# Kernel optimization log

Measured on AMD Instinct MI355X. Metric: run time of the kernel, lower is better.

The kernel has to match this reference:

```python
import jax, jax.numpy as jnp
import numpy as np

B, N, D, BS = 2, 4096, 2048, 256  # batch, seq, d_model, chunk size


def rms_norm(x):
    eps = jnp.asarray(jnp.finfo(x.dtype).eps, x.dtype)
    return x * jax.lax.rsqrt(jnp.mean(x * x, axis=-1, keepdims=True) + eps)


def la_kernel(q, k, v, bs):
    # chunked linear attention: intra-chunk masked QK^T + cross-chunk KV recurrence
    b, n, d = q.shape
    T = n // bs
    qc = q.reshape(b, T, bs, d).transpose(1, 0, 2, 3)  # [T,B,bs,d]
    kc = k.reshape(b, T, bs, d).transpose(1, 0, 2, 3)
    vc = v.reshape(b, T, bs, d).transpose(1, 0, 2, 3)
    mask = jnp.tril(jnp.ones((bs, bs), q.dtype))

    def step(kv, qkv):
        qt, kt, vt = qkv  # each [B,bs,d]
        s = jnp.einsum('bid,bjd->bij', qt, kt) * mask        # masked intra-chunk scores
        ot = jnp.einsum('bij,bjd->bid', s, vt) + jnp.einsum('bid,bde->bie', qt, kv)
        kv = kv + jnp.einsum('bjd,bje->bde', kt, vt)          # state update AFTER output
        return kv, ot

    kv0 = jnp.zeros((b, d, d), q.dtype)
    _, o = jax.lax.scan(step, kv0, (qc, kc, vc))              # o: [T,B,bs,d]
    return o.transpose(1, 0, 2, 3).reshape(b, n, d)


def setup_inputs() -> dict:
    key = jax.random.key(0)
    ks = jax.random.split(key, 6)
    scale = 0.02
    x = jax.random.normal(ks[0], (B, N, D), jnp.float32)
    Wq = jax.random.normal(ks[1], (D, D), jnp.float32) * scale
    Wk = jax.random.normal(ks[2], (D, D), jnp.float32) * scale
    Wv = jax.random.normal(ks[3], (D, D), jnp.float32) * scale
    Wg = jax.random.normal(ks[4], (D, D), jnp.float32) * scale
    Wp = jax.random.normal(ks[5], (D, D), jnp.float32) * scale
    return {'x': x, 'Wq': Wq, 'Wk': Wk, 'Wv': Wv, 'Wg': Wg, 'Wp': Wp}


def reference(x, Wq, Wk, Wv, Wg, Wp):
    # weights stored torch-style (out,in): y = x @ W^T
    xn = rms_norm(x)
    q = jax.nn.silu(jnp.einsum('bnd,od->bno', xn, Wq))
    k = jax.nn.silu(jnp.einsum('bnd,od->bno', xn, Wk))
    v = jax.nn.silu(jnp.einsum('bnd,od->bno', xn, Wv))
    g = jax.nn.sigmoid(jnp.einsum('bnd,od->bno', xn, Wg))
    o = la_kernel(q, k, v, BS) * g
    return jnp.einsum('bnd,od->bno', o, Wp)
```

## Files before the change

### kernel.cpp

```cpp
#include <hip/hip_runtime.h>
#include <hip/hip_bf16.h>

typedef __bf16 bf16;
typedef __bf16 bf16x4 __attribute__((ext_vector_type(4)));
typedef __bf16 bf16x8 __attribute__((ext_vector_type(8)));
typedef float f32x4 __attribute__((ext_vector_type(4)));
typedef unsigned int u32;

#define D_    2048
#define NSEQ  4096
#define BATCH 2
#define CH    1024
#define TC    4
#define MROWS 8192

__device__ __forceinline__ void gload16(const bf16* g, bf16* l) {
  __builtin_amdgcn_global_load_lds(
      (const __attribute__((address_space(1))) u32*)g,
      (__attribute__((address_space(3))) u32*)l, 16, 0, 0);
}


struct SmemTiles {
  alignas(16) bf16 As[2][128 * 32];
  alignas(16) bf16 Bs[2][128 * 32];
};

__device__ __forceinline__ void stage128(SmemTiles& sm, int bb, const bf16* A,
                                         int lda, const bf16* B, int ldb,
                                         int k0, int tid) {
#pragma unroll
  for (int it = 0; it < 2; ++it) {
    int c = it * 256 + tid;
    int r = c >> 2;
    int co = (c & 3) << 3;
    gload16(A + (size_t)r * lda + k0 + co, &sm.As[bb][c * 8]);
    gload16(B + (size_t)r * ldb + k0 + co, &sm.Bs[bb][c * 8]);
  }
}

__device__ __forceinline__ void gemm_core(SmemTiles& sm, const bf16* A, int lda,
                                          const bf16* B, int ldb, int K,
                                          f32x4 acc[4][4]) {
  const int tid = threadIdx.x;
  const int lane = tid & 63;
  const int wave = tid >> 6;
  const int wr = wave >> 1, wc = wave & 1;
  const int l15 = lane & 15, kl = lane >> 4;
  const int NT = K >> 5;
  if (NT <= 0) return;

  stage128(sm, 0, A, lda, B, ldb, 0, tid);
  __syncthreads();

  const int ao = (wr * 64 + l15) * 32 + kl * 8;
  const int bo = (wc * 64 + l15) * 32 + kl * 8;

  for (int t = 0; t < NT; ++t) {
    if (t + 1 < NT)
      stage128(sm, (t + 1) & 1, A, lda, B, ldb, (t + 1) * 32, tid);
    const bf16* Ab = sm.As[t & 1];
    const bf16* Bb = sm.Bs[t & 1];
    bf16x8 a[4], b[4];
#pragma unroll
    for (int m = 0; m < 4; ++m) a[m] = *(const bf16x8*)(Ab + ao + m * 16 * 32);
#pragma unroll
    for (int n = 0; n < 4; ++n) b[n] = *(const bf16x8*)(Bb + bo + n * 16 * 32);
    __builtin_amdgcn_s_setprio(1);
#pragma unroll
    for (int m = 0; m < 4; ++m)
#pragma unroll
      for (int n = 0; n < 4; ++n)
        acc[m][n] = __builtin_amdgcn_mfma_f32_16x16x32_bf16(a[m], b[n], acc[m][n], 0, 0, 0);
    __builtin_amdgcn_s_setprio(0);
    if (t + 1 < NT) __syncthreads();
  }
}

#define EPILOGUE_VARS                              \
  const int lane = threadIdx.x & 63;               \
  const int wave = threadIdx.x >> 6;               \
  const int wr = wave >> 1, wc = wave & 1;         \
  const int l15 = lane & 15, kl = lane >> 4;


struct SmemW {
  alignas(16) bf16 A[2][128 * 32];
  alignas(16) bf16 B[2][256 * 32];
};

__device__ __forceinline__ void stageW(SmemW& sm, int bb, const bf16* A,
                                       int lda, const bf16* B, int ldb,
                                       int k0, int wave, int lane) {
  const int r16 = lane & 15, c8 = lane >> 4;
  gload16(A + (size_t)(wave * 16 + r16) * lda + k0 + c8 * 8,
          &sm.A[bb][wave * 512 + lane * 8]);
#pragma unroll
  for (int j = 0; j < 2; ++j) {
    int nb = 2 * wave + j;
    gload16(B + (size_t)(nb * 16 + r16) * ldb + k0 + c8 * 8,
            &sm.B[bb][nb * 512 + lane * 8]);
  }
}

__device__ __forceinline__ void gemmW_core(SmemW& sm, const bf16* A, int lda,
                                           const bf16* B, int ldb, int K,
                                           f32x4 acc[4][4]) {
  const int tid = threadIdx.x;
  const int wave = tid >> 6, lane = tid & 63;
  const int wr = wave >> 2, wc = wave & 3;
  const int NT = K >> 5;
  if (NT <= 0) return;

  stageW(sm, 0, A, lda, B, ldb, 0, wave, lane);
  if (NT > 1) {
    stageW(sm, 1, A, lda, B, ldb, 32, wave, lane);
    asm volatile("s_waitcnt vmcnt(3)" ::: "memory");
  } else {
    asm volatile("s_waitcnt vmcnt(0)" ::: "memory");
  }
  __builtin_amdgcn_s_barrier();

  const int aoff = wr * 2048 + lane * 8;
  const int boff = wc * 2048 + lane * 8;

  for (int t = 0; t < NT; ++t) {
    const bf16* Ab = sm.A[t & 1];
    const bf16* Bb = sm.B[t & 1];
    bf16x8 av[4], bv[4];
#pragma unroll
    for (int m = 0; m < 4; ++m) av[m] = *(const bf16x8*)&Ab[aoff + m * 512];
#pragma unroll
    for (int n = 0; n < 4; ++n) bv[n] = *(const bf16x8*)&Bb[boff + n * 512];
    asm volatile("s_waitcnt lgkmcnt(0)" ::: "memory");
    __builtin_amdgcn_s_barrier();
    if (t + 2 < NT)
      stageW(sm, t & 1, A, lda, B, ldb, (t + 2) * 32, wave, lane);
    __builtin_amdgcn_s_setprio(1);
#pragma unroll
    for (int m = 0; m < 4; ++m)
#pragma unroll
      for (int n = 0; n < 4; ++n)
        acc[m][n] = __builtin_amdgcn_mfma_f32_16x16x32_bf16(av[m], bv[n],
                                                            acc[m][n], 0, 0, 0);
    __builtin_amdgcn_s_setprio(0);
    if (t + 1 < NT) {
      if (t + 2 < NT)
        asm volatile("s_waitcnt vmcnt(3)" ::: "memory");
      else
        asm volatile("s_waitcnt vmcnt(0)" ::: "memory");
      __builtin_amdgcn_s_barrier();
    }
  }
}

#define EPILOGUEW_VARS                             \
  const int lane = threadIdx.x & 63;               \
  const int wave = threadIdx.x >> 6;               \
  const int wr = wave >> 2, wc = wave & 3;         \
  const int l15 = lane & 15, kl = lane >> 4;

__device__ __forceinline__ void swzW(int& bx, int& by) {
  int lin = blockIdx.y * gridDim.x + blockIdx.x;
  int xcd = lin & 7, pos = lin >> 3;
  by = xcd * 8 + (pos >> 3);
  bx = pos & 7;
}


__global__ __launch_bounds__(256) void k_f2b(const float* __restrict__ in,
                                             bf16* __restrict__ out) {
  int i = (blockIdx.x * 256 + threadIdx.x) * 8;
  float4 a = *(const float4*)(in + i);
  float4 b = *(const float4*)(in + i + 4);
  bf16x8 o;
  o[0] = (bf16)a.x; o[1] = (bf16)a.y; o[2] = (bf16)a.z; o[3] = (bf16)a.w;
  o[4] = (bf16)b.x; o[5] = (bf16)b.y; o[6] = (bf16)b.z; o[7] = (bf16)b.w;
  *(bf16x8*)(out + i) = o;
}

__global__ __launch_bounds__(256) void k_f2b2(const float* __restrict__ in0,
                                              const float* __restrict__ in1,
                                              bf16* __restrict__ out) {
  int i = (blockIdx.x * 256 + threadIdx.x) * 8;
  const float* src = (i < D_ * D_) ? in0 : in1;
  int off = (i < D_ * D_) ? i : i - D_ * D_;
  float4 a = *(const float4*)(src + off);
  float4 b = *(const float4*)(src + off + 4);
  bf16x8 o;
  o[0] = (bf16)a.x; o[1] = (bf16)a.y; o[2] = (bf16)a.z; o[3] = (bf16)a.w;
  o[4] = (bf16)b.x; o[5] = (bf16)b.y; o[6] = (bf16)b.z; o[7] = (bf16)b.w;
  *(bf16x8*)(out + i) = o;
}

__global__ __launch_bounds__(256) void k_rms(const float* __restrict__ x,
                                             bf16* __restrict__ xn) {
  const int row = blockIdx.x;
  const int tid = threadIdx.x;
  const float* xr = x + (size_t)row * D_;
  float4 a = *(const float4*)(xr + tid * 8);
  float4 b = *(const float4*)(xr + tid * 8 + 4);
  float ss = a.x * a.x + a.y * a.y + a.z * a.z + a.w * a.w +
             b.x * b.x + b.y * b.y + b.z * b.z + b.w * b.w;
#pragma unroll
  for (int o = 32; o > 0; o >>= 1) ss += __shfl_xor(ss, o, 64);
  __shared__ float red[4];
  if ((tid & 63) == 0) red[tid >> 6] = ss;
  __syncthreads();
  float tot = red[0] + red[1] + red[2] + red[3];
  float sc = rsqrtf(tot * (1.f / D_) + 1.1920928955078125e-07f);
  bf16x8 o;
  o[0] = (bf16)(a.x * sc); o[1] = (bf16)(a.y * sc);
  o[2] = (bf16)(a.z * sc); o[3] = (bf16)(a.w * sc);
  o[4] = (bf16)(b.x * sc); o[5] = (bf16)(b.y * sc);
  o[6] = (bf16)(b.z * sc); o[7] = (bf16)(b.w * sc);
  *(bf16x8*)(xn + (size_t)row * D_ + tid * 8) = o;
}


template <int ACT, int SMODE>
__global__ __launch_bounds__(512, 4) void k_proj2(const bf16* __restrict__ xn,
                                                  const bf16* __restrict__ W,
                                                  bf16* __restrict__ Cn,
                                                  bf16* __restrict__ Ct) {
  __shared__ SmemW sm;
  int bx, by;
  swzW(bx, by);
  const int row0 = by * 128, col0 = bx * 256;
  f32x4 acc[4][4] = {};
  gemmW_core(sm, xn + (size_t)row0 * D_, D_, W + (size_t)col0 * D_, D_, D_, acc);
  EPILOGUEW_VARS
#pragma unroll
  for (int m = 0; m < 4; ++m)
#pragma unroll
    for (int n = 0; n < 4; ++n) {
      const int rb = row0 + wr * 64 + m * 16 + kl * 4;
      const int c = col0 + wc * 64 + n * 16 + l15;
      bf16 ob[4];
#pragma unroll
      for (int j = 0; j < 4; ++j) {
        float v = acc[m][n][j];
        if (ACT == 1) v = v / (1.f + __expf(-v));
        if (ACT == 2) v = 1.f / (1.f + __expf(-v));
        ob[j] = (bf16)v;
      }
      if (SMODE & 1) {
#pragma unroll
        for (int j = 0; j < 4; ++j) Cn[(size_t)(rb + j) * D_ + c] = ob[j];
      }
      if (SMODE & 2) {
        bf16x4 tv = {ob[0], ob[1], ob[2], ob[3]};
        *(bf16x4*)&Ct[((size_t)(rb >> 12) * D_ + c) * NSEQ + (rb & (NSEQ - 1))] = tv;
      }
    }
}

__global__ __launch_bounds__(512, 4) void k_final2(const bf16* __restrict__ og,
                                                   const bf16* __restrict__ Wp,
                                                   float* __restrict__ out) {
  __shared__ SmemW sm;
  int bx, by;
  swzW(bx, by);
  const int row0 = by * 128, col0 = bx * 256;
  f32x4 acc[4][4] = {};
  gemmW_core(sm, og + (size_t)row0 * D_, D_, Wp + (size_t)col0 * D_, D_, D_, acc);
  EPILOGUEW_VARS
#pragma unroll
  for (int m = 0; m < 4; ++m)
#pragma unroll
    for (int n = 0; n < 4; ++n)
#pragma unroll
      for (int j = 0; j < 4; ++j) {
        int r = row0 + wr * 64 + m * 16 + kl * 4 + j;
        int c = col0 + wc * 64 + n * 16 + l15;
        out[(size_t)r * D_ + c] = acc[m][n][j];
      }
}


__global__ __launch_bounds__(256) void k_scores(const bf16* __restrict__ q,
                                                const bf16* __restrict__ k,
                                                bf16* __restrict__ s) {
  const int z = blockIdx.z, b = z >> 2, t = z & 3;
  const int row0 = blockIdx.y * 128, col0 = blockIdx.x * 128;
  if (col0 > row0) return;
  __shared__ SmemTiles sm;
  f32x4 acc[4][4] = {};
  gemm_core(sm, q + (size_t)(b * NSEQ + t * CH + row0) * D_, D_,
                k + (size_t)(b * NSEQ + t * CH + col0) * D_, D_, D_, acc);
  EPILOGUE_VARS
  bf16* sp = s + (size_t)z * CH * CH;
#pragma unroll
  for (int m = 0; m < 4; ++m)
#pragma unroll
    for (int n = 0; n < 4; ++n)
#pragma unroll
      for (int j = 0; j < 4; ++j) {
        int i = row0 + wr * 64 + m * 16 + kl * 4 + j;
        int jc = col0 + wc * 64 + n * 16 + l15;
        float v = (i >= jc) ? acc[m][n][j] : 0.f;
        sp[(size_t)i * CH + jc] = (bf16)v;
      }
}

__global__ __launch_bounds__(256) void k_ointra(const bf16* __restrict__ s,
                                                const bf16* __restrict__ vT,
                                                const bf16* __restrict__ g,
                                                bf16* __restrict__ og) {
  __shared__ SmemTiles sm;
  const int z = blockIdx.z, b = z >> 2, t = z & 3;
  const int row0 = blockIdx.y * 128, col0 = blockIdx.x * 128;
  const int K = row0 + 128;
  f32x4 acc[4][4] = {};
  gemm_core(sm, s + (size_t)z * CH * CH + (size_t)row0 * CH, CH,
                vT + (size_t)b * D_ * NSEQ + (size_t)col0 * NSEQ + t * CH, NSEQ,
                K, acc);
  EPILOGUE_VARS
  const bool gate0 = (t == 0);
#pragma unroll
  for (int m = 0; m < 4; ++m)
#pragma unroll
    for (int n = 0; n < 4; ++n)
#pragma unroll
      for (int j = 0; j < 4; ++j) {
        int i = row0 + wr * 64 + m * 16 + kl * 4 + j;
        int c = col0 + wc * 64 + n * 16 + l15;
        size_t idx = (size_t)(b * NSEQ + t * CH + i) * D_ + c;
        float v = acc[m][n][j];
        if (gate0) v *= (float)g[idx];
        og[idx] = (bf16)v;
      }
}

__global__ __launch_bounds__(256) void k_ointer(const bf16* __restrict__ q,
                                                const bf16* __restrict__ kvb,
                                                const bf16* __restrict__ g,
                                                bf16* __restrict__ og, int t) {
  __shared__ SmemTiles sm;
  const int b = blockIdx.z;
  const int row0 = blockIdx.y * 128, col0 = blockIdx.x * 128;
  f32x4 acc[4][4] = {};
  gemm_core(sm, q + (size_t)(b * NSEQ + t * CH + row0) * D_, D_,
                kvb + (size_t)b * D_ * D_ + (size_t)col0 * D_, D_, D_, acc);
  EPILOGUE_VARS
#pragma unroll
  for (int m = 0; m < 4; ++m)
#pragma unroll
    for (int n = 0; n < 4; ++n)
#pragma unroll
      for (int j = 0; j < 4; ++j) {
        int i = row0 + wr * 64 + m * 16 + kl * 4 + j;
        int c = col0 + wc * 64 + n * 16 + l15;
        size_t idx = (size_t)(b * NSEQ + t * CH + i) * D_ + c;
        float v = ((float)og[idx] + acc[m][n][j]) * (float)g[idx];
        og[idx] = (bf16)v;
      }
}

__global__ __launch_bounds__(256) void k_update(const bf16* __restrict__ vT,
                                                const bf16* __restrict__ kT,
                                                bf16* __restrict__ kvb, int t) {
  __shared__ SmemTiles sm;
  const int b = blockIdx.z;
  const int row0 = blockIdx.y * 128, col0 = blockIdx.x * 128;
  f32x4 acc[4][4] = {};
  gemm_core(sm, vT + (size_t)b * D_ * NSEQ + (size_t)row0 * NSEQ + t * CH, NSEQ,
                kT + (size_t)b * D_ * NSEQ + (size_t)col0 * NSEQ + t * CH, NSEQ,
                CH, acc);
  EPILOGUE_VARS
#pragma unroll
  for (int m = 0; m < 4; ++m)
#pragma unroll
    for (int n = 0; n < 4; ++n)
#pragma unroll
      for (int j = 0; j < 4; ++j) {
        int e = row0 + wr * 64 + m * 16 + kl * 4 + j;
        int d = col0 + wc * 64 + n * 16 + l15;
        size_t idx = (size_t)b * D_ * D_ + (size_t)e * D_ + d;
        float v = acc[m][n][j];
        if (t > 0) v += (float)kvb[idx];
        kvb[idx] = (bf16)v;
      }
}


extern "C" void kernel_launch(void* const* d_in, const int* in_sizes, int n_in,
                              void* d_out, int out_size, void* d_ws, size_t ws_size,
                              hipStream_t stream) {
  (void)in_sizes; (void)n_in; (void)out_size; (void)ws_size;
  const float* x  = (const float*)d_in[0];
  const float* Wq = (const float*)d_in[1];
  const float* Wk = (const float*)d_in[2];
  const float* Wv = (const float*)d_in[3];
  const float* Wg = (const float*)d_in[4];
  const float* Wp = (const float*)d_in[5];
  float* out = (float*)d_out;

  char* p = (char*)d_ws;
  auto take = [&](size_t bytes) {
    char* r = p;
    p += (bytes + 255) & ~(size_t)255;
    return r;
  };
  const size_t MD2 = (size_t)MROWS * D_ * 2;

  bf16* xn  = (bf16*)take(MD2);
  bf16* kT  = (bf16*)take(MD2);
  bf16* vT  = (bf16*)take(MD2);
  bf16* k   = (bf16*)take((size_t)MROWS * D_ * 2);
  char* shared = take((size_t)BATCH * TC * CH * CH * 2);
  bf16* Wpair = (bf16*)shared;
  bf16* s    = (bf16*)shared;
  bf16* kvb  = (bf16*)shared;
  bf16* og = xn;

  bf16* q = (bf16*)d_out;
  bf16* g = (bf16*)d_out + (size_t)MROWS * D_;

  const size_t W1 = (size_t)D_ * D_;
  dim3 gpW(D_ / 256, MROWS / 128);

  k_rms<<<MROWS, 256, 0, stream>>>(x, xn);

  k_f2b2<<<2 * (D_ * D_) / 2048, 256, 0, stream>>>(Wq, Wk, Wpair);
  k_proj2<1, 1><<<gpW, 512, 0, stream>>>(xn, Wpair, q, (bf16*)nullptr);
  k_proj2<1, 3><<<gpW, 512, 0, stream>>>(xn, Wpair + W1, k, kT);
  k_f2b2<<<2 * (D_ * D_) / 2048, 256, 0, stream>>>(Wv, Wg, Wpair);
  k_proj2<1, 2><<<gpW, 512, 0, stream>>>(xn, Wpair, (bf16*)nullptr, vT);
  k_proj2<2, 1><<<gpW, 512, 0, stream>>>(xn, Wpair + W1, g, (bf16*)nullptr);

  k_scores<<<dim3(CH / 128, CH / 128, BATCH * TC), 256, 0, stream>>>(q, k, s);
  k_ointra<<<dim3(D_ / 128, CH / 128, BATCH * TC), 256, 0, stream>>>(s, vT, g, og);

  for (int t = 1; t < TC; ++t) {
    k_update<<<dim3(D_ / 128, D_ / 128, BATCH), 256, 0, stream>>>(vT, kT,
                                                                  kvb, t - 1);
    k_ointer<<<dim3(D_ / 128, CH / 128, BATCH), 256, 0, stream>>>(q, kvb, g,
                                                                  og, t);
  }

  bf16* Wpb = (bf16*)shared;
  k_f2b<<<(D_ * D_) / 2048, 256, 0, stream>>>(Wp, Wpb);
  k_final2<<<gpW, 512, 0, stream>>>(og, Wpb, out);
}
```

Measured before the change: 847.0 us.

## Batch per-chunk KV updates and inter-chunk outputs into single launches with prefix sums

Replaces the serial loop of alternating KV-state update and inter-chunk output GEMMs with one launch that computes all three chunk KV outer products in parallel. Two small elementwise add kernels then form the prefix sums, and one launch computes every chunk's inter-chunk contribution. This removes the serial dependency chain and the small-grid launches, giving more blocks per launch for better GPU occupancy. The trade-off is extra memory traffic from the add kernels and workspace reuse of the k buffer for the KV states.

```diff
diff --git a/kernel.cpp b/kernel.cpp
--- a/kernel.cpp
+++ b/kernel.cpp
@@ -193,6 +193,17 @@
   *(bf16x8*)(out + i) = o;
 }
 
+__global__ __launch_bounds__(256) void k_add(bf16* __restrict__ dst,
+                                             const bf16* __restrict__ src) {
+  size_t i = ((size_t)blockIdx.x * 256 + threadIdx.x) * 8;
+  bf16x8 a = *(const bf16x8*)(dst + i);
+  bf16x8 b = *(const bf16x8*)(src + i);
+  bf16x8 o;
+#pragma unroll
+  for (int j = 0; j < 8; ++j) o[j] = (bf16)((float)a[j] + (float)b[j]);
+  *(bf16x8*)(dst + i) = o;
+}
+
 __global__ __launch_bounds__(256) void k_rms(const float* __restrict__ x,
                                              bf16* __restrict__ xn) {
   const int row = blockIdx.x;
@@ -332,16 +343,46 @@
       }
 }
 
-__global__ __launch_bounds__(256) void k_ointer(const bf16* __restrict__ q,
-                                                const bf16* __restrict__ kvb,
-                                                const bf16* __restrict__ g,
-                                                bf16* __restrict__ og, int t) {
+__global__ __launch_bounds__(256) void k_update_all(const bf16* __restrict__ vT,
+                                                    const bf16* __restrict__ kT,
+                                                    bf16* __restrict__ kv01,
+                                                    bf16* __restrict__ kv2) {
   __shared__ SmemTiles sm;
-  const int b = blockIdx.z;
+  const int z = blockIdx.z, s = z >> 1, b = z & 1;
   const int row0 = blockIdx.y * 128, col0 = blockIdx.x * 128;
   f32x4 acc[4][4] = {};
+  gemm_core(sm, vT + (size_t)b * D_ * NSEQ + (size_t)row0 * NSEQ + s * CH, NSEQ,
+                kT + (size_t)b * D_ * NSEQ + (size_t)col0 * NSEQ + s * CH, NSEQ,
+                CH, acc);
+  EPILOGUE_VARS
+  bf16* dst = (s < 2) ? kv01 + (size_t)(s * 2 + b) * D_ * D_
+                      : kv2 + (size_t)b * D_ * D_;
+#pragma unroll
+  for (int m = 0; m < 4; ++m)
+#pragma unroll
+    for (int n = 0; n < 4; ++n)
+#pragma unroll
+      for (int j = 0; j < 4; ++j) {
+        int e = row0 + wr * 64 + m * 16 + kl * 4 + j;
+        int d = col0 + wc * 64 + n * 16 + l15;
+        dst[(size_t)e * D_ + d] = (bf16)acc[m][n][j];
+      }
+}
+
+__global__ __launch_bounds__(256) void k_ointer_all(const bf16* __restrict__ q,
+                                                    const bf16* __restrict__ kv01,
+                                                    const bf16* __restrict__ kv2,
+                                                    const bf16* __restrict__ g,
+                                                    bf16* __restrict__ og) {
+  __shared__ SmemTiles sm;
+  const int z = blockIdx.z;
+  const int t = (z >> 1) + 1, b = z & 1;
+  const bf16* kv = (t <= 2) ? kv01 + (size_t)((t - 1) * 2 + b) * D_ * D_
+                            : kv2 + (size_t)b * D_ * D_;
+  const int row0 = blockIdx.y * 128, col0 = blockIdx.x * 128;
+  f32x4 acc[4][4] = {};
   gemm_core(sm, q + (size_t)(b * NSEQ + t * CH + row0) * D_, D_,
-                kvb + (size_t)b * D_ * D_ + (size_t)col0 * D_, D_, D_, acc);
+                kv + (size_t)col0 * D_, D_, D_, acc);
   EPILOGUE_VARS
 #pragma unroll
   for (int m = 0; m < 4; ++m)
@@ -354,32 +395,6 @@
         size_t idx = (size_t)(b * NSEQ + t * CH + i) * D_ + c;
         float v = ((float)og[idx] + acc[m][n][j]) * (float)g[idx];
         og[idx] = (bf16)v;
-      }
-}
-
-__global__ __launch_bounds__(256) void k_update(const bf16* __restrict__ vT,
-                                                const bf16* __restrict__ kT,
-                                                bf16* __restrict__ kvb, int t) {
-  __shared__ SmemTiles sm;
-  const int b = blockIdx.z;
-  const int row0 = blockIdx.y * 128, col0 = blockIdx.x * 128;
-  f32x4 acc[4][4] = {};
-  gemm_core(sm, vT + (size_t)b * D_ * NSEQ + (size_t)row0 * NSEQ + t * CH, NSEQ,
-                kT + (size_t)b * D_ * NSEQ + (size_t)col0 * NSEQ + t * CH, NSEQ,
-                CH, acc);
-  EPILOGUE_VARS
-#pragma unroll
-  for (int m = 0; m < 4; ++m)
-#pragma unroll
-    for (int n = 0; n < 4; ++n)
-#pragma unroll
-      for (int j = 0; j < 4; ++j) {
-        int e = row0 + wr * 64 + m * 16 + kl * 4 + j;
-        int d = col0 + wc * 64 + n * 16 + l15;
-        size_t idx = (size_t)b * D_ * D_ + (size_t)e * D_ + d;
-        float v = acc[m][n][j];
-        if (t > 0) v += (float)kvb[idx];
-        kvb[idx] = (bf16)v;
       }
 }
 
@@ -403,15 +418,18 @@
     return r;
   };
   const size_t MD2 = (size_t)MROWS * D_ * 2;
+  const size_t KV1 = (size_t)D_ * D_;
 
   bf16* xn  = (bf16*)take(MD2);
   bf16* kT  = (bf16*)take(MD2);
   bf16* vT  = (bf16*)take(MD2);
-  bf16* k   = (bf16*)take((size_t)MROWS * D_ * 2);
+  char* kregion = take(MD2);
+  bf16* k    = (bf16*)kregion;
+  bf16* kv01 = (bf16*)kregion;
   char* shared = take((size_t)BATCH * TC * CH * CH * 2);
   bf16* Wpair = (bf16*)shared;
   bf16* s    = (bf16*)shared;
-  bf16* kvb  = (bf16*)shared;
+  bf16* kv2  = (bf16*)shared;
   bf16* og = xn;
 
   bf16* q = (bf16*)d_out;
@@ -432,12 +450,11 @@
   k_scores<<<dim3(CH / 128, CH / 128, BATCH * TC), 256, 0, stream>>>(q, k, s);
   k_ointra<<<dim3(D_ / 128, CH / 128, BATCH * TC), 256, 0, stream>>>(s, vT, g, og);
 
-  for (int t = 1; t < TC; ++t) {
-    k_update<<<dim3(D_ / 128, D_ / 128, BATCH), 256, 0, stream>>>(vT, kT,
-                                                                  kvb, t - 1);
-    k_ointer<<<dim3(D_ / 128, CH / 128, BATCH), 256, 0, stream>>>(q, kvb, g,
-                                                                  og, t);
-  }
+  k_update_all<<<dim3(D_ / 128, D_ / 128, 6), 256, 0, stream>>>(vT, kT, kv01, kv2);
+  k_add<<<(2 * D_ * D_) / 2048, 256, 0, stream>>>(kv01 + 2 * KV1, kv01);
+  k_add<<<(2 * D_ * D_) / 2048, 256, 0, stream>>>(kv2, kv01 + 2 * KV1);
+  k_ointer_all<<<dim3(D_ / 128, CH / 128, 6), 256, 0, stream>>>(q, kv01, kv2,
+                                                                g, og);
 
   bf16* Wpb = (bf16*)shared;
   k_f2b<<<(D_ * D_) / 2048, 256, 0, stream>>>(Wp, Wpb);
```

Result: faster. 769.1 us (-9.2%).
